# Optimization experiments

Measured on AMD Instinct MI355X. Metric: run time of the kernel, lower is better.

## Reference

```python
import jax, jax.numpy as jnp
import numpy as np

THETA = 10000.0

def precompute_freqs_cis(dim, seq_len):
    freqs = 1.0 / THETA ** (jnp.arange(0, dim, 2)[: dim // 2].astype(jnp.float32) / dim)
    t = jnp.arange(seq_len, dtype=jnp.float32)
    ang = jnp.outer(t, freqs)  # [T, dim/2]
    return jax.lax.complex(jnp.cos(ang), jnp.sin(ang))

def apply_rope(x, freqs_cis):
    # x: [..., T, D]; freqs_cis: [T, D/2] complex
    xr = x.astype(jnp.float32).reshape(*x.shape[:-1], -1, 2)
    xc = jax.lax.complex(xr[..., 0], xr[..., 1]) * freqs_cis
    out = jnp.stack([jnp.real(xc), jnp.imag(xc)], axis=-1).reshape(x.shape)
    return out.astype(x.dtype)

def setup_inputs() -> dict:
    key = jax.random.key(0)
    k1, k2, k3, k4 = jax.random.split(key, 4)
    B, T, E, DQ, DV = 4, 2048, 1024, 128, 128
    s = 1.0 / np.sqrt(E)
    return {
        "embedding_word": jax.random.normal(k1, (B, T, E), dtype=jnp.float32),
        "w_Q": jax.random.normal(k2, (DQ, E), dtype=jnp.float32) * s,  # torch Linear weight [out,in]
        "w_K": jax.random.normal(k3, (DQ, E), dtype=jnp.float32) * s,
        "w_V": jax.random.normal(k4, (DV, E), dtype=jnp.float32) * s,
    }

def reference(embedding_word, w_Q, w_K, w_V):
    T = embedding_word.shape[-2]
    dq = w_Q.shape[0]
    q = jnp.einsum("bte,de->btd", embedding_word, w_Q)
    k = jnp.einsum("bte,de->btd", embedding_word, w_K)
    v = jnp.einsum("bte,de->btd", embedding_word, w_V)
    fc = precompute_freqs_cis(dq, T)
    q = apply_rope(q, fc)
    k = apply_rope(k, fc)
    scores = jnp.einsum("bqd,bkd->bqk", q, k)
    causal = jnp.triu(jnp.ones((T, T), dtype=bool), k=1)
    masked = jnp.where(causal, -jnp.inf, scores)
    weights = jax.nn.softmax(masked / jnp.sqrt(jnp.float32(dq)), axis=-1)
    return jnp.einsum("bqk,bkd->bqd", weights, v)
```

## Files before the change

### kernel.cpp

```cpp
#include <hip/hip_runtime.h>
#include <math.h>


#define B_ 4
#define T_ 2048
#define E_ 1024
#define D_ 128
#define BT_ (B_ * T_)

#define UNITS_PER_B 160
#define UNITS (UNITS_PER_B * B_)

typedef __bf16 bf16_t;
typedef __bf16 bf16x4 __attribute__((ext_vector_type(4)));
typedef __bf16 bf16x8 __attribute__((ext_vector_type(8)));
typedef float f32x4 __attribute__((ext_vector_type(4)));

#define GLD16(g, l)                                                         \
  __builtin_amdgcn_global_load_lds(                                         \
      (const __attribute__((address_space(1))) void*)(g),                   \
      (__attribute__((address_space(3))) void*)(l), 16, 0, 0)

__global__ __launch_bounds__(256) void precast_kernel(
    const float* __restrict__ X, const float* __restrict__ Wq,
    const float* __restrict__ Wk, const float* __restrict__ Wv,
    bf16_t* __restrict__ Xb, bf16_t* __restrict__ Wb,
    float2* __restrict__ Tab) {
  const int XC = BT_ * E_ / 8;
  const int WC = 3 * D_ * E_ / 8;
  for (int c = blockIdx.x * 256 + threadIdx.x; c < XC + WC;
       c += gridDim.x * 256) {
    const float* src;
    bf16_t* dst;
    if (c < XC) {
      src = X + (size_t)c * 8;
      dst = Xb + (size_t)c * 8;
    } else {
      const int cw = c - XC;
      const int z = cw / (D_ * E_ / 8);
      const int r = cw % (D_ * E_ / 8);
      src = ((z == 0) ? Wq : (z == 1) ? Wk : Wv) + (size_t)r * 8;
      dst = Wb + (size_t)z * D_ * E_ + (size_t)r * 8;
    }
    float4 u = *(const float4*)src;
    float4 v = *(const float4*)(src + 4);
    bf16x8 t;
    t[0] = (bf16_t)u.x; t[1] = (bf16_t)u.y; t[2] = (bf16_t)u.z; t[3] = (bf16_t)u.w;
    t[4] = (bf16_t)v.x; t[5] = (bf16_t)v.y; t[6] = (bf16_t)v.z; t[7] = (bf16_t)v.w;
    *(bf16x8*)dst = t;
  }
  const float NLOG_ = -0.14391156514261485f;
  for (int idx = blockIdx.x * 256 + threadIdx.x; idx < T_ * 64;
       idx += gridDim.x * 256) {
    const int t = idx >> 6, j = idx & 63;
    const float freq = expf(NLOG_ * (float)j);
    float sn, cs;
    sincosf((float)t * freq, &sn, &cs);
    Tab[idx] = make_float2(cs, sn);
  }
}

__global__ __launch_bounds__(256) void proj64_kernel(
    const bf16_t* __restrict__ Xb, const bf16_t* __restrict__ Wb,
    const float2* __restrict__ Tab, bf16_t* __restrict__ Qws,
    bf16_t* __restrict__ Kws, bf16_t* __restrict__ Vtws) {
  const int o = blockIdx.x;
  const int ell = (o & 7) * 96 + (o >> 3);
  const int mt = ell / 6, ny = ell % 6;
  const int bt0 = mt * 64;

  const int tid = threadIdx.x;
  const int lane = tid & 63;
  const int wv = tid >> 6;
  const int wr = wv >> 1, wc = wv & 1;
  const int g = lane >> 4, lm = lane & 15;

  __shared__ bf16_t Ab[2][64 * 64];
  __shared__ bf16_t Bb[2][64 * 64];

  const bf16_t* Wz = Wb + (size_t)ny * 64 * E_;

  f32x4 acc[2][2];
#pragma unroll
  for (int m = 0; m < 2; m++)
#pragma unroll
    for (int n = 0; n < 2; n++) acc[m][n] = 0.0f;

  auto stage = [&](int t, int bf) {
    const int k0 = t * 64;
#pragma unroll
    for (int j = 0; j < 2; j++) {
      const int cb = (wv * 2 + j) * 64;
      const int c = cb + lane;
      const int row = c >> 3;
      const int eoff = ((c & 7) * 8) ^ ((row & 7) << 3);
      GLD16(Xb + (size_t)(bt0 + row) * E_ + k0 + eoff, &Ab[bf][cb * 8]);
    }
#pragma unroll
    for (int j = 0; j < 2; j++) {
      const int cb = (wv * 2 + j) * 64;
      const int c = cb + lane;
      const int row = c >> 3;
      const int eoff = ((c & 7) * 8) ^ ((row & 7) << 3);
      GLD16(Wz + (size_t)row * E_ + k0 + eoff, &Bb[bf][cb * 8]);
    }
  };

  auto compute = [&](int bf) {
#pragma unroll
    for (int ks = 0; ks < 2; ks++) {
      bf16x8 a0, a1, b0, b1;
      {
        const int r0 = wr * 32 + lm;
        a0 = *(const bf16x8*)&Ab[bf][r0 * 64 + ((ks * 32 + g * 8) ^ ((r0 & 7) << 3))];
        const int r1 = wr * 32 + 16 + lm;
        a1 = *(const bf16x8*)&Ab[bf][r1 * 64 + ((ks * 32 + g * 8) ^ ((r1 & 7) << 3))];
        const int s0 = wc * 32 + lm;
        b0 = *(const bf16x8*)&Bb[bf][s0 * 64 + ((ks * 32 + g * 8) ^ ((s0 & 7) << 3))];
        const int s1 = wc * 32 + 16 + lm;
        b1 = *(const bf16x8*)&Bb[bf][s1 * 64 + ((ks * 32 + g * 8) ^ ((s1 & 7) << 3))];
      }
      acc[0][0] = __builtin_amdgcn_mfma_f32_16x16x32_bf16(a0, b0, acc[0][0], 0, 0, 0);
      acc[0][1] = __builtin_amdgcn_mfma_f32_16x16x32_bf16(a0, b1, acc[0][1], 0, 0, 0);
      acc[1][0] = __builtin_amdgcn_mfma_f32_16x16x32_bf16(a1, b0, acc[1][0], 0, 0, 0);
      acc[1][1] = __builtin_amdgcn_mfma_f32_16x16x32_bf16(a1, b1, acc[1][1], 0, 0, 0);
    }
  };

  stage(0, 0);
  __syncthreads();
  int cur = 0;
  for (int t = 0; t < 16; t++) {
    if (t < 15) stage(t + 1, cur ^ 1);
    compute(cur);
    __syncthreads();
    cur ^= 1;
  }

  const int b = bt0 >> 11;
#pragma unroll
  for (int nf = 0; nf < 2; nf++) {
    const int col = ny * 64 + wc * 32 + nf * 16 + lm;
    const int z = col >> 7;
    const int d = col & 127;
#pragma unroll
    for (int mf = 0; mf < 2; mf++) {
      const int row0 = bt0 + wr * 32 + mf * 16 + g * 4;
      if (z < 2) {
        bf16_t* dst = (z == 0) ? Qws : Kws;
#pragma unroll
        for (int r = 0; r < 4; r++) {
          const int bt = row0 + r;
          const int tt = bt & (T_ - 1);
          float val = acc[mf][nf][r];
          float prt = __shfl_xor(val, 1, 64);
          const float2 cs = Tab[(size_t)tt * 64 + (d >> 1)];
          const float outv =
              (d & 1) ? (prt * cs.y + val * cs.x) : (val * cs.x - prt * cs.y);
          dst[(size_t)bt * D_ + d] = (bf16_t)outv;
        }
      } else {
        bf16x4 pv;
#pragma unroll
        for (int r = 0; r < 4; r++) pv[r] = (bf16_t)acc[mf][nf][r];
        const int tt0 = row0 & (T_ - 1);
        *(bf16x4*)&Vtws[((size_t)(b * D_ + d)) * T_ + tt0] = pv;
      }
    }
  }
}

__global__ __launch_bounds__(128) void attn_part_kernel(
    const bf16_t* __restrict__ Qws, const bf16_t* __restrict__ Kws,
    const bf16_t* __restrict__ Vtws, float* __restrict__ Opart,
    float* __restrict__ Mpart, float* __restrict__ Lpart) {
  const int idx = blockIdx.x;
  const int b = idx / UNITS_PER_B;
  const int rem = idx % UNITS_PER_B;
  int qi, ci;
  if (rem < 16) { qi = rem; ci = 0; }
  else if (rem < 48) { int r2 = rem - 16; qi = 16 + (r2 >> 1); ci = r2 & 1; }
  else if (rem < 96) { int r2 = rem - 48; qi = 32 + r2 / 3; ci = r2 % 3; }
  else { int r2 = rem - 96; qi = 48 + (r2 >> 2); ci = r2 & 3; }
  const int slot = idx;

  const int q0 = qi * 32;
  const int tiles = (qi >> 1) + 1;
  const int t0 = ci * 8;
  const int t1 = min(t0 + 8, tiles);

  const int tid = threadIdx.x;
  const int lane = tid & 63;
  const int wv = tid >> 6;
  const int g = lane >> 4;
  const int lm = lane & 15;

  __shared__ bf16_t Ks[64 * 136];
  __shared__ bf16_t Vts[128 * 72];
  __shared__ bf16_t Ps[2 * 16 * 72];

  bf16x8 qf[4];
  {
    const bf16_t* qb = Qws + (size_t)(b * T_ + q0 + wv * 16 + lm) * D_;
#pragma unroll
    for (int kc = 0; kc < 4; kc++) qf[kc] = *(const bf16x8*)(qb + kc * 32 + g * 8);
  }

  f32x4 o[8];
#pragma unroll
  for (int i = 0; i < 8; i++) o[i] = 0.0f;
  float m_r[4], l_r[4];
#pragma unroll
  for (int r = 0; r < 4; r++) { m_r[r] = -1e30f; l_r[r] = 0.0f; }
  const float sc = 0.08838834764831845f;

  bf16x8 kreg[8], vreg[8];
  auto load_tiles = [&](int it) {
    const int k0 = it * 64;
#pragma unroll
    for (int i = 0; i < 8; i++) {
      const int c = tid + i * 128;
      kreg[i] = *(const bf16x8*)(Kws + (size_t)(b * T_ + k0 + (c >> 4)) * D_ +
                                 (c & 15) * 8);
    }
#pragma unroll
    for (int i = 0; i < 8; i++) {
      const int c = tid + i * 128;
      vreg[i] = *(const bf16x8*)(Vtws + (size_t)(b * D_ + (c >> 3)) * T_ + k0 +
                                 (c & 7) * 8);
    }
  };
  auto write_lds = [&]() {
#pragma unroll
    for (int i = 0; i < 8; i++) {
      const int c = tid + i * 128;
      *(bf16x8*)&Ks[(c >> 4) * 136 + (c & 15) * 8] = kreg[i];
    }
#pragma unroll
    for (int i = 0; i < 8; i++) {
      const int c = tid + i * 128;
      *(bf16x8*)&Vts[(c >> 3) * 72 + (c & 7) * 8] = vreg[i];
    }
  };

  load_tiles(t0);
  for (int it = t0; it < t1; it++) {
    write_lds();
    __syncthreads();
    if (it + 1 < t1) load_tiles(it + 1);

    const int k0 = it * 64;
    f32x4 s[4];
#pragma unroll
    for (int nb = 0; nb < 4; nb++) s[nb] = 0.0f;
#pragma unroll
    for (int nb = 0; nb < 4; nb++) {
#pragma unroll
      for (int kc = 0; kc < 4; kc++) {
        bf16x8 bk = *(const bf16x8*)&Ks[(nb * 16 + lm) * 136 + kc * 32 + g * 8];
        s[nb] = __builtin_amdgcn_mfma_f32_16x16x32_bf16(qf[kc], bk, s[nb], 0, 0, 0);
      }
    }

    const bool diag = (it == tiles - 1);
#pragma unroll
    for (int r = 0; r < 4; r++) {
      const int qrow = q0 + wv * 16 + g * 4 + r;
      float sv[4];
#pragma unroll
      for (int nb = 0; nb < 4; nb++) {
        sv[nb] = s[nb][r] * sc;
        if (diag && (k0 + nb * 16 + lm > qrow)) sv[nb] = -1e30f;
      }
      float tm = fmaxf(fmaxf(sv[0], sv[1]), fmaxf(sv[2], sv[3]));
      tm = fmaxf(tm, __shfl_xor(tm, 1, 64));
      tm = fmaxf(tm, __shfl_xor(tm, 2, 64));
      tm = fmaxf(tm, __shfl_xor(tm, 4, 64));
      tm = fmaxf(tm, __shfl_xor(tm, 8, 64));
      const float mnew = fmaxf(m_r[r], tm);
      const float alpha = __expf(m_r[r] - mnew);
      float p[4], rs = 0.0f;
#pragma unroll
      for (int nb = 0; nb < 4; nb++) { p[nb] = __expf(sv[nb] - mnew); rs += p[nb]; }
      rs += __shfl_xor(rs, 1, 64);
      rs += __shfl_xor(rs, 2, 64);
      rs += __shfl_xor(rs, 4, 64);
      rs += __shfl_xor(rs, 8, 64);
      l_r[r] = l_r[r] * alpha + rs;
      m_r[r] = mnew;
#pragma unroll
      for (int nb2 = 0; nb2 < 8; nb2++) o[nb2][r] *= alpha;
#pragma unroll
      for (int nb = 0; nb < 4; nb++)
        Ps[wv * 1152 + (g * 4 + r) * 72 + nb * 16 + lm] = (bf16_t)p[nb];
    }

    bf16x8 pa0 = *(const bf16x8*)&Ps[wv * 1152 + lm * 72 + g * 8];
    bf16x8 pa1 = *(const bf16x8*)&Ps[wv * 1152 + lm * 72 + 32 + g * 8];
#pragma unroll
    for (int nb2 = 0; nb2 < 8; nb2++) {
      bf16x8 bv0 = *(const bf16x8*)&Vts[(nb2 * 16 + lm) * 72 + g * 8];
      o[nb2] = __builtin_amdgcn_mfma_f32_16x16x32_bf16(pa0, bv0, o[nb2], 0, 0, 0);
      bf16x8 bv1 = *(const bf16x8*)&Vts[(nb2 * 16 + lm) * 72 + 32 + g * 8];
      o[nb2] = __builtin_amdgcn_mfma_f32_16x16x32_bf16(pa1, bv1, o[nb2], 0, 0, 0);
    }
    __syncthreads();
  }

#pragma unroll
  for (int r = 0; r < 4; r++) {
    const int row = wv * 16 + g * 4 + r;
    if (lm == 0) {
      Mpart[slot * 32 + row] = m_r[r];
      Lpart[slot * 32 + row] = l_r[r];
    }
    float* dst = Opart + ((size_t)slot * 32 + row) * D_;
#pragma unroll
    for (int nb2 = 0; nb2 < 8; nb2++) dst[nb2 * 16 + lm] = o[nb2][r];
  }
}

__global__ __launch_bounds__(256) void attn_combine_kernel(
    const float* __restrict__ Opart, const float* __restrict__ Mpart,
    const float* __restrict__ Lpart, float* __restrict__ Out) {
  const int qi = blockIdx.x;
  const int b = blockIdx.y;
  const int gg = qi >> 4;
  const int nc = gg + 1;
  const int base = b * UNITS_PER_B + ((gg * (gg + 1)) / 2) * 16 + (qi & 15) * nc;
  const int t = threadIdx.x;
  const int row = t >> 3;
  const int d0 = (t & 7) * 16;

  float mv[4];
  float mmax = -1e30f;
  for (int ci = 0; ci < nc; ci++) {
    mv[ci] = Mpart[(base + ci) * 32 + row];
    mmax = fmaxf(mmax, mv[ci]);
  }
  f32x4 acc[4];
#pragma unroll
  for (int j = 0; j < 4; j++) acc[j] = 0.0f;
  float l = 0.0f;
  for (int ci = 0; ci < nc; ci++) {
    const float w = __expf(mv[ci] - mmax);
    l += w * Lpart[(base + ci) * 32 + row];
    const float* op = Opart + ((size_t)(base + ci) * 32 + row) * D_ + d0;
#pragma unroll
    for (int j = 0; j < 4; j++) {
      float4 v = *(const float4*)(op + j * 4);
      acc[j][0] += w * v.x; acc[j][1] += w * v.y;
      acc[j][2] += w * v.z; acc[j][3] += w * v.w;
    }
  }
  const float inv = 1.0f / l;
  float* dst = Out + ((size_t)(b * T_ + qi * 32 + row)) * D_ + d0;
#pragma unroll
  for (int j = 0; j < 4; j++) {
    float4 v;
    v.x = acc[j][0] * inv; v.y = acc[j][1] * inv;
    v.z = acc[j][2] * inv; v.w = acc[j][3] * inv;
    *(float4*)(dst + j * 4) = v;
  }
}

__global__ __launch_bounds__(256) void proj_rope_kernel(
    const float* __restrict__ X, const float* __restrict__ Wq,
    const float* __restrict__ Wk, const float* __restrict__ Wv,
    bf16_t* __restrict__ Qws, bf16_t* __restrict__ Kws,
    bf16_t* __restrict__ Vtws) {
  const int z = blockIdx.y;
  const float* __restrict__ W = (z == 0) ? Wq : (z == 1) ? Wk : Wv;
  const int bt0 = blockIdx.x * 64;
  const int tid = threadIdx.x;
  const int lane = tid & 63;
  const int wv = tid >> 6;
  const int g = lane >> 4;
  const int lm = lane & 15;

  __shared__ bf16_t Xs[64 * 40];
  __shared__ bf16_t Ws[128 * 40];

  f32x4 acc[8];
#pragma unroll
  for (int i = 0; i < 8; i++) acc[i] = 0.0f;

  for (int kk = 0; kk < E_ / 32; kk++) {
    {
      const int row = tid >> 2, c0 = (tid & 3) * 8;
      const float* src = X + (size_t)(bt0 + row) * E_ + kk * 32 + c0;
      float4 u = *(const float4*)src;
      float4 v = *(const float4*)(src + 4);
      bf16x8 t;
      t[0] = (bf16_t)u.x; t[1] = (bf16_t)u.y; t[2] = (bf16_t)u.z; t[3] = (bf16_t)u.w;
      t[4] = (bf16_t)v.x; t[5] = (bf16_t)v.y; t[6] = (bf16_t)v.z; t[7] = (bf16_t)v.w;
      *(bf16x8*)&Xs[row * 40 + c0] = t;
    }
#pragma unroll
    for (int h = 0; h < 2; h++) {
      const int cc = tid * 2 + h;
      const int row = cc >> 2, c0 = (cc & 3) * 8;
      const float* src = W + (size_t)row * E_ + kk * 32 + c0;
      float4 u = *(const float4*)src;
      float4 v = *(const float4*)(src + 4);
      bf16x8 t;
      t[0] = (bf16_t)u.x; t[1] = (bf16_t)u.y; t[2] = (bf16_t)u.z; t[3] = (bf16_t)u.w;
      t[4] = (bf16_t)v.x; t[5] = (bf16_t)v.y; t[6] = (bf16_t)v.z; t[7] = (bf16_t)v.w;
      *(bf16x8*)&Ws[row * 40 + c0] = t;
    }
    __syncthreads();
    bf16x8 a = *(const bf16x8*)&Xs[(wv * 16 + lm) * 40 + g * 8];
#pragma unroll
    for (int nb = 0; nb < 8; nb++) {
      bf16x8 bb = *(const bf16x8*)&Ws[(nb * 16 + lm) * 40 + g * 8];
      acc[nb] = __builtin_amdgcn_mfma_f32_16x16x32_bf16(a, bb, acc[nb], 0, 0, 0);
    }
    __syncthreads();
  }
  const float NLOG_ = -0.14391156514261485f;
#pragma unroll
  for (int nb = 0; nb < 8; nb++) {
    const int col = nb * 16 + lm;
    const float freq = expf(NLOG_ * (float)(col >> 1));
#pragma unroll
    for (int r = 0; r < 4; r++) {
      const int bt = bt0 + wv * 16 + g * 4 + r;
      float val = acc[nb][r];
      float prt = __shfl_xor(val, 1, 64);
      if (z < 2) {
        const int t = bt & (T_ - 1);
        const float ang = (float)t * freq;
        float sn, cs;
        sincosf(ang, &sn, &cs);
        const float outv = (col & 1) ? (prt * sn + val * cs) : (val * cs - prt * sn);
        bf16_t* dst = (z == 0) ? Qws : Kws;
        dst[(size_t)bt * D_ + col] = (bf16_t)outv;
      } else {
        const int b = bt >> 11, t = bt & (T_ - 1);
        Vtws[((size_t)(b * D_ + col)) * T_ + t] = (bf16_t)val;
      }
    }
  }
}

__global__ __launch_bounds__(128) void attn_kernel(
    const bf16_t* __restrict__ Qws, const bf16_t* __restrict__ Kws,
    const bf16_t* __restrict__ Vtws, float* __restrict__ Out) {
  const int b = blockIdx.y;
  const int qi = blockIdx.x;
  const int q0 = qi * 32;
  const int tid = threadIdx.x;
  const int lane = tid & 63;
  const int wv = tid >> 6;
  const int g = lane >> 4;
  const int lm = lane & 15;

  __shared__ bf16_t Ks[32 * 136];
  __shared__ bf16_t Vts[128 * 40];
  __shared__ bf16_t Ps[2 * 16 * 40];

  bf16x8 qf[4];
  {
    const bf16_t* qb = Qws + (size_t)(b * T_ + q0 + wv * 16 + lm) * D_;
#pragma unroll
    for (int kk = 0; kk < 4; kk++) qf[kk] = *(const bf16x8*)(qb + kk * 32 + g * 8);
  }
  f32x4 o[8];
#pragma unroll
  for (int i = 0; i < 8; i++) o[i] = 0.0f;
  float m_r[4], l_r[4];
#pragma unroll
  for (int r = 0; r < 4; r++) { m_r[r] = -1e30f; l_r[r] = 0.0f; }
  const float sc = 0.08838834764831845f;

  for (int kt = 0; kt <= qi; kt++) {
    const int kv0 = kt * 32;
#pragma unroll
    for (int i = 0; i < 4; i++) {
      const int c = tid + i * 128;
      const int row = c >> 4, part = c & 15;
      bf16x8 v = *(const bf16x8*)(Kws + (size_t)(b * T_ + kv0 + row) * D_ + part * 8);
      *(bf16x8*)&Ks[row * 136 + part * 8] = v;
    }
#pragma unroll
    for (int i = 0; i < 4; i++) {
      const int c = tid + i * 128;
      const int d = c >> 2, part = c & 3;
      bf16x8 v = *(const bf16x8*)(Vtws + (size_t)(b * D_ + d) * T_ + kv0 + part * 8);
      *(bf16x8*)&Vts[d * 40 + part * 8] = v;
    }
    __syncthreads();
    f32x4 s[2];
    s[0] = 0.0f; s[1] = 0.0f;
#pragma unroll
    for (int nb = 0; nb < 2; nb++) {
#pragma unroll
      for (int kc = 0; kc < 4; kc++) {
        bf16x8 bk = *(const bf16x8*)&Ks[(nb * 16 + lm) * 136 + kc * 32 + g * 8];
        s[nb] = __builtin_amdgcn_mfma_f32_16x16x32_bf16(qf[kc], bk, s[nb], 0, 0, 0);
      }
    }
    const bool diag = (kt == qi);
#pragma unroll
    for (int r = 0; r < 4; r++) {
      float sv0 = s[0][r] * sc;
      float sv1 = s[1][r] * sc;
      if (diag) {
        const int rowr = wv * 16 + g * 4 + r;
        if (lm > rowr) sv0 = -1e30f;
        if (lm + 16 > rowr) sv1 = -1e30f;
      }
      float tm = fmaxf(sv0, sv1);
      tm = fmaxf(tm, __shfl_xor(tm, 1, 64));
      tm = fmaxf(tm, __shfl_xor(tm, 2, 64));
      tm = fmaxf(tm, __shfl_xor(tm, 4, 64));
      tm = fmaxf(tm, __shfl_xor(tm, 8, 64));
      const float mnew = fmaxf(m_r[r], tm);
      const float alpha = __expf(m_r[r] - mnew);
      const float p0 = __expf(sv0 - mnew);
      const float p1 = __expf(sv1 - mnew);
      float rs = p0 + p1;
      rs += __shfl_xor(rs, 1, 64);
      rs += __shfl_xor(rs, 2, 64);
      rs += __shfl_xor(rs, 4, 64);
      rs += __shfl_xor(rs, 8, 64);
      l_r[r] = l_r[r] * alpha + rs;
      m_r[r] = mnew;
#pragma unroll
      for (int nb2 = 0; nb2 < 8; nb2++) o[nb2][r] *= alpha;
      Ps[wv * 640 + (g * 4 + r) * 40 + lm] = (bf16_t)p0;
      Ps[wv * 640 + (g * 4 + r) * 40 + 16 + lm] = (bf16_t)p1;
    }
    bf16x8 pa = *(const bf16x8*)&Ps[wv * 640 + lm * 40 + g * 8];
#pragma unroll
    for (int nb2 = 0; nb2 < 8; nb2++) {
      bf16x8 bv = *(const bf16x8*)&Vts[(nb2 * 16 + lm) * 40 + g * 8];
      o[nb2] = __builtin_amdgcn_mfma_f32_16x16x32_bf16(pa, bv, o[nb2], 0, 0, 0);
    }
    __syncthreads();
  }
#pragma unroll
  for (int r = 0; r < 4; r++) {
    const float inv = 1.0f / l_r[r];
    float* dst = Out + (size_t)(b * T_ + q0 + wv * 16 + g * 4 + r) * D_;
#pragma unroll
    for (int nb2 = 0; nb2 < 8; nb2++) dst[nb2 * 16 + lm] = o[nb2][r] * inv;
  }
}

extern "C" void kernel_launch(void* const* d_in, const int* in_sizes, int n_in,
                              void* d_out, int out_size, void* d_ws,
                              size_t ws_size, hipStream_t stream) {
  const float* X = (const float*)d_in[0];
  const float* Wq = (const float*)d_in[1];
  const float* Wk = (const float*)d_in[2];
  const float* Wv = (const float*)d_in[3];
  float* Out = (float*)d_out;

  const size_t xb_bytes = (size_t)BT_ * E_ * sizeof(bf16_t);
  const size_t wb_bytes = (size_t)3 * D_ * E_ * sizeof(bf16_t);
  const size_t qkv_bytes = (size_t)3 * BT_ * D_ * sizeof(bf16_t);
  const size_t opart_bytes = (size_t)UNITS * 32 * D_ * sizeof(float);
  const size_t ml_bytes = (size_t)UNITS * 32 * sizeof(float);
  const size_t tab_bytes = (size_t)T_ * 64 * sizeof(float2);

  const size_t needA =
      xb_bytes + wb_bytes + qkv_bytes + opart_bytes + 2 * ml_bytes + tab_bytes;
  const size_t needB = qkv_bytes + opart_bytes + 2 * ml_bytes;

  if (ws_size >= needA) {
    bf16_t* Xb = (bf16_t*)d_ws;
    bf16_t* Wb = Xb + (size_t)BT_ * E_;
    bf16_t* Qws = Wb + (size_t)3 * D_ * E_;
    bf16_t* Kws = Qws + (size_t)BT_ * D_;
    bf16_t* Vtws = Kws + (size_t)BT_ * D_;
    float* Opart = (float*)((char*)d_ws + xb_bytes + wb_bytes + qkv_bytes);
    float* Mpart = (float*)((char*)Opart + opart_bytes);
    float* Lpart = (float*)((char*)Mpart + ml_bytes);
    float2* Tab = (float2*)((char*)Lpart + ml_bytes);

    hipLaunchKernelGGL(precast_kernel, dim3(2048), dim3(256), 0, stream,
                       X, Wq, Wk, Wv, Xb, Wb, Tab);
    hipLaunchKernelGGL(proj64_kernel, dim3(768), dim3(256), 0, stream,
                       Xb, Wb, Tab, Qws, Kws, Vtws);
    hipLaunchKernelGGL(attn_part_kernel, dim3(UNITS), dim3(128), 0, stream,
                       Qws, Kws, Vtws, Opart, Mpart, Lpart);
    hipLaunchKernelGGL(attn_combine_kernel, dim3(T_ / 32, B_), dim3(256), 0,
                       stream, Opart, Mpart, Lpart, Out);
  } else if (ws_size >= needB) {
    bf16_t* Qws = (bf16_t*)d_ws;
    bf16_t* Kws = Qws + (size_t)BT_ * D_;
    bf16_t* Vtws = Kws + (size_t)BT_ * D_;
    float* Opart = (float*)((char*)d_ws + qkv_bytes);
    float* Mpart = (float*)((char*)Opart + opart_bytes);
    float* Lpart = (float*)((char*)Mpart + ml_bytes);
    hipLaunchKernelGGL(proj_rope_kernel, dim3(BT_ / 64, 3), dim3(256), 0,
                       stream, X, Wq, Wk, Wv, Qws, Kws, Vtws);
    hipLaunchKernelGGL(attn_part_kernel, dim3(UNITS), dim3(128), 0, stream,
                       Qws, Kws, Vtws, Opart, Mpart, Lpart);
    hipLaunchKernelGGL(attn_combine_kernel, dim3(T_ / 32, B_), dim3(256), 0,
                       stream, Opart, Mpart, Lpart, Out);
  } else {
    bf16_t* Qws = (bf16_t*)d_ws;
    bf16_t* Kws = Qws + (size_t)BT_ * D_;
    bf16_t* Vtws = Kws + (size_t)BT_ * D_;
    hipLaunchKernelGGL(proj_rope_kernel, dim3(BT_ / 64, 3), dim3(256), 0,
                       stream, X, Wq, Wk, Wv, Qws, Kws, Vtws);
    hipLaunchKernelGGL(attn_kernel, dim3(T_ / 32, B_), dim3(128), 0, stream,
                       Qws, Kws, Vtws, Out);
  }
}
```

Before: 62.42 us.

## Replace LDS-staged projection GEMM with per-wave register-tiled direct-load kernel

The projection GEMM no longer stages tiles through LDS with block-wide barriers. Each wave now computes a 64x48 output tile, loading MFMA operands straight from global memory into registers with two-stage register double-buffering, on a swizzled 256-block grid. The precast kernel is restructured so each block converts 32 contiguous rows of X with a matching swizzle, and the launch drops from 2048 to 256 blocks. This removes LDS traffic and synchronisation, at the cost of no cross-wave operand sharing (more L2/global reads per FLOP), higher register pressure, and fewer blocks in flight.

```diff
diff --git a/kernel.cpp b/kernel.cpp
--- a/kernel.cpp
+++ b/kernel.cpp
@@ -16,42 +16,45 @@
 typedef __bf16 bf16x8 __attribute__((ext_vector_type(8)));
 typedef float f32x4 __attribute__((ext_vector_type(4)));
 
-#define GLD16(g, l)                                                         \
-  __builtin_amdgcn_global_load_lds(                                         \
-      (const __attribute__((address_space(1))) void*)(g),                   \
-      (__attribute__((address_space(3))) void*)(l), 16, 0, 0)
-
 __global__ __launch_bounds__(256) void precast_kernel(
     const float* __restrict__ X, const float* __restrict__ Wq,
     const float* __restrict__ Wk, const float* __restrict__ Wv,
     bf16_t* __restrict__ Xb, bf16_t* __restrict__ Wb,
     float2* __restrict__ Tab) {
-  const int XC = BT_ * E_ / 8;
-  const int WC = 3 * D_ * E_ / 8;
-  for (int c = blockIdx.x * 256 + threadIdx.x; c < XC + WC;
-       c += gridDim.x * 256) {
-    const float* src;
-    bf16_t* dst;
-    if (c < XC) {
-      src = X + (size_t)c * 8;
-      dst = Xb + (size_t)c * 8;
-    } else {
-      const int cw = c - XC;
-      const int z = cw / (D_ * E_ / 8);
-      const int r = cw % (D_ * E_ / 8);
-      src = ((z == 0) ? Wq : (z == 1) ? Wk : Wv) + (size_t)r * 8;
-      dst = Wb + (size_t)z * D_ * E_ + (size_t)r * 8;
-    }
+  const int o = blockIdx.x;
+  const int swz = (o & 7) * 32 + (o >> 3);
+  const int r0 = swz * 32;
+  const int tid = threadIdx.x;
+
+#pragma unroll 4
+  for (int i = 0; i < 16; i++) {
+    const int c = tid + i * 256;
+    const int row = r0 + (c >> 7);
+    const int ch = (c & 127) * 8;
+    const float* src = X + (size_t)row * E_ + ch;
     float4 u = *(const float4*)src;
     float4 v = *(const float4*)(src + 4);
     bf16x8 t;
     t[0] = (bf16_t)u.x; t[1] = (bf16_t)u.y; t[2] = (bf16_t)u.z; t[3] = (bf16_t)u.w;
     t[4] = (bf16_t)v.x; t[5] = (bf16_t)v.y; t[6] = (bf16_t)v.z; t[7] = (bf16_t)v.w;
-    *(bf16x8*)dst = t;
-  }
+    *(bf16x8*)(Xb + (size_t)row * E_ + ch) = t;
+  }
+
+  const int gidx = o * 256 + tid;
+  if (gidx < 3 * D_ * E_ / 8) {
+    const int z = gidx / 16384;
+    const int r = gidx % 16384;
+    const float* src = ((z == 0) ? Wq : (z == 1) ? Wk : Wv) + (size_t)r * 8;
+    float4 u = *(const float4*)src;
+    float4 v = *(const float4*)(src + 4);
+    bf16x8 t;
+    t[0] = (bf16_t)u.x; t[1] = (bf16_t)u.y; t[2] = (bf16_t)u.z; t[3] = (bf16_t)u.w;
+    t[4] = (bf16_t)v.x; t[5] = (bf16_t)v.y; t[6] = (bf16_t)v.z; t[7] = (bf16_t)v.w;
+    *(bf16x8*)(Wb + (size_t)z * D_ * E_ + (size_t)r * 8) = t;
+  }
+
   const float NLOG_ = -0.14391156514261485f;
-  for (int idx = blockIdx.x * 256 + threadIdx.x; idx < T_ * 64;
-       idx += gridDim.x * 256) {
+  for (int idx = gidx; idx < T_ * 64; idx += 65536) {
     const int t = idx >> 6, j = idx & 63;
     const float freq = expf(NLOG_ * (float)j);
     float sn, cs;
@@ -60,92 +63,76 @@
   }
 }
 
-__global__ __launch_bounds__(256) void proj64_kernel(
+__global__ __launch_bounds__(256) void proj_lf_kernel(
     const bf16_t* __restrict__ Xb, const bf16_t* __restrict__ Wb,
     const float2* __restrict__ Tab, bf16_t* __restrict__ Qws,
     bf16_t* __restrict__ Kws, bf16_t* __restrict__ Vtws) {
   const int o = blockIdx.x;
-  const int ell = (o & 7) * 96 + (o >> 3);
-  const int mt = ell / 6, ny = ell % 6;
-  const int bt0 = mt * 64;
-
-  const int tid = threadIdx.x;
-  const int lane = tid & 63;
-  const int wv = tid >> 6;
-  const int wr = wv >> 1, wc = wv & 1;
+  const int swz = (o & 7) * 32 + (o >> 3);
+  const int wv = threadIdx.x >> 6;
+  const int w = swz * 4 + wv;
+  const int mb = w >> 3;
+  const int cbnd = w & 7;
+  const int m0 = mb * 64;
+  const int c0 = cbnd * 48;
+  const int lane = threadIdx.x & 63;
   const int g = lane >> 4, lm = lane & 15;
 
-  __shared__ bf16_t Ab[2][64 * 64];
-  __shared__ bf16_t Bb[2][64 * 64];
-
-  const bf16_t* Wz = Wb + (size_t)ny * 64 * E_;
-
-  f32x4 acc[2][2];
-#pragma unroll
-  for (int m = 0; m < 2; m++)
-#pragma unroll
-    for (int n = 0; n < 2; n++) acc[m][n] = 0.0f;
-
-  auto stage = [&](int t, int bf) {
-    const int k0 = t * 64;
-#pragma unroll
-    for (int j = 0; j < 2; j++) {
-      const int cb = (wv * 2 + j) * 64;
-      const int c = cb + lane;
-      const int row = c >> 3;
-      const int eoff = ((c & 7) * 8) ^ ((row & 7) << 3);
-      GLD16(Xb + (size_t)(bt0 + row) * E_ + k0 + eoff, &Ab[bf][cb * 8]);
-    }
-#pragma unroll
-    for (int j = 0; j < 2; j++) {
-      const int cb = (wv * 2 + j) * 64;
-      const int c = cb + lane;
-      const int row = c >> 3;
-      const int eoff = ((c & 7) * 8) ^ ((row & 7) << 3);
-      GLD16(Wz + (size_t)row * E_ + k0 + eoff, &Bb[bf][cb * 8]);
-    }
-  };
-
-  auto compute = [&](int bf) {
-#pragma unroll
-    for (int ks = 0; ks < 2; ks++) {
-      bf16x8 a0, a1, b0, b1;
-      {
-        const int r0 = wr * 32 + lm;
-        a0 = *(const bf16x8*)&Ab[bf][r0 * 64 + ((ks * 32 + g * 8) ^ ((r0 & 7) << 3))];
-        const int r1 = wr * 32 + 16 + lm;
-        a1 = *(const bf16x8*)&Ab[bf][r1 * 64 + ((ks * 32 + g * 8) ^ ((r1 & 7) << 3))];
-        const int s0 = wc * 32 + lm;
-        b0 = *(const bf16x8*)&Bb[bf][s0 * 64 + ((ks * 32 + g * 8) ^ ((s0 & 7) << 3))];
-        const int s1 = wc * 32 + 16 + lm;
-        b1 = *(const bf16x8*)&Bb[bf][s1 * 64 + ((ks * 32 + g * 8) ^ ((s1 & 7) << 3))];
-      }
-      acc[0][0] = __builtin_amdgcn_mfma_f32_16x16x32_bf16(a0, b0, acc[0][0], 0, 0, 0);
-      acc[0][1] = __builtin_amdgcn_mfma_f32_16x16x32_bf16(a0, b1, acc[0][1], 0, 0, 0);
-      acc[1][0] = __builtin_amdgcn_mfma_f32_16x16x32_bf16(a1, b0, acc[1][0], 0, 0, 0);
-      acc[1][1] = __builtin_amdgcn_mfma_f32_16x16x32_bf16(a1, b1, acc[1][1], 0, 0, 0);
-    }
-  };
-
-  stage(0, 0);
-  __syncthreads();
-  int cur = 0;
-  for (int t = 0; t < 16; t++) {
-    if (t < 15) stage(t + 1, cur ^ 1);
-    compute(cur);
-    __syncthreads();
-    cur ^= 1;
-  }
-
-  const int b = bt0 >> 11;
-#pragma unroll
-  for (int nf = 0; nf < 2; nf++) {
-    const int col = ny * 64 + wc * 32 + nf * 16 + lm;
+  const bf16_t* aP = Xb + (size_t)(m0 + lm) * E_ + g * 8;
+  const bf16_t* bP = Wb + (size_t)(c0 + lm) * E_ + g * 8;
+
+  f32x4 acc[4][3];
+#pragma unroll
+  for (int mf = 0; mf < 4; mf++)
+#pragma unroll
+    for (int nf = 0; nf < 3; nf++) acc[mf][nf] = 0.0f;
+
+  bf16x8 aA[4], bA[3], aB[4], bB[3];
+#pragma unroll
+  for (int mf = 0; mf < 4; mf++) aA[mf] = *(const bf16x8*)(aP + mf * 16 * E_);
+#pragma unroll
+  for (int nf = 0; nf < 3; nf++) bA[nf] = *(const bf16x8*)(bP + nf * 16 * E_);
+
+  for (int kk = 0; kk < 32; kk += 2) {
+    const int off1 = (kk + 1) * 32;
+#pragma unroll
+    for (int mf = 0; mf < 4; mf++)
+      aB[mf] = *(const bf16x8*)(aP + mf * 16 * E_ + off1);
+#pragma unroll
+    for (int nf = 0; nf < 3; nf++)
+      bB[nf] = *(const bf16x8*)(bP + nf * 16 * E_ + off1);
+#pragma unroll
+    for (int mf = 0; mf < 4; mf++)
+#pragma unroll
+      for (int nf = 0; nf < 3; nf++)
+        acc[mf][nf] =
+            __builtin_amdgcn_mfma_f32_16x16x32_bf16(aA[mf], bA[nf], acc[mf][nf], 0, 0, 0);
+    if (kk + 2 < 32) {
+      const int off2 = (kk + 2) * 32;
+#pragma unroll
+      for (int mf = 0; mf < 4; mf++)
+        aA[mf] = *(const bf16x8*)(aP + mf * 16 * E_ + off2);
+#pragma unroll
+      for (int nf = 0; nf < 3; nf++)
+        bA[nf] = *(const bf16x8*)(bP + nf * 16 * E_ + off2);
+    }
+#pragma unroll
+    for (int mf = 0; mf < 4; mf++)
+#pragma unroll
+      for (int nf = 0; nf < 3; nf++)
+        acc[mf][nf] =
+            __builtin_amdgcn_mfma_f32_16x16x32_bf16(aB[mf], bB[nf], acc[mf][nf], 0, 0, 0);
+  }
+
+  const int b = m0 >> 11;
+#pragma unroll
+  for (int nf = 0; nf < 3; nf++) {
+    const int col = c0 + nf * 16 + lm;
     const int z = col >> 7;
     const int d = col & 127;
 #pragma unroll
-    for (int mf = 0; mf < 2; mf++) {
-      const int row0 = bt0 + wr * 32 + mf * 16 + g * 4;
+    for (int mf = 0; mf < 4; mf++) {
+      const int row0 = m0 + mf * 16 + g * 4;
       if (z < 2) {
         bf16_t* dst = (z == 0) ? Qws : Kws;
 #pragma unroll
@@ -579,9 +566,9 @@
     float* Lpart = (float*)((char*)Mpart + ml_bytes);
     float2* Tab = (float2*)((char*)Lpart + ml_bytes);
 
-    hipLaunchKernelGGL(precast_kernel, dim3(2048), dim3(256), 0, stream,
+    hipLaunchKernelGGL(precast_kernel, dim3(256), dim3(256), 0, stream,
                        X, Wq, Wk, Wv, Xb, Wb, Tab);
-    hipLaunchKernelGGL(proj64_kernel, dim3(768), dim3(256), 0, stream,
+    hipLaunchKernelGGL(proj_lf_kernel, dim3(256), dim3(256), 0, stream,
                        Xb, Wb, Tab, Qws, Kws, Vtws);
     hipLaunchKernelGGL(attn_part_kernel, dim3(UNITS), dim3(128), 0, stream,
                        Qws, Kws, Vtws, Opart, Mpart, Lpart);
```

Result: slower. 77.12 us (+23.6%).
